# Optimization experiments

Hardware: AMD Instinct MI355X
Metric: run time of the kernel (lower is better)

The kernel has to match this reference:

```python
import jax, jax.numpy as jnp
from jax import lax
import numpy as np

B, T, UMAX, D = 32, 128, 64, 512
U1 = UMAX + 1
BLANK = D - 1  # blank=-1 -> last vocab slot
NEG = -1e30    # finite -inf surrogate (keeps logaddexp grads NaN-free)


def setup_inputs() -> dict:
    key = jax.random.key(0)
    k1, k2, k3, k4 = jax.random.split(key, 4)
    logits = jax.random.normal(k1, (B, T, U1, D), dtype=jnp.float32)
    logit_lengths = jax.random.randint(k2, (B,), T // 2, T + 1, dtype=jnp.int32)
    target_lengths = jax.random.randint(k3, (B,), UMAX // 2, UMAX + 1, dtype=jnp.int32)
    targets = jax.random.randint(k4, (B, UMAX), 0, D - 1, dtype=jnp.int32)  # never blank
    return {"logits": logits, "logit_lengths": logit_lengths,
            "target_lengths": target_lengths, "targets": targets}


def _transducer_costs(log_probs, logit_lengths, target_lengths, targets):
    """RNN-T alpha DP; costs[b] = -(alpha[T_b-1, U_b] + lp_blank[T_b-1, U_b])."""
    b, t_max, u1, d = log_probs.shape
    lp_blank = log_probs[..., BLANK]                                   # [B,T,U1]
    tgt_pad = jnp.concatenate([targets, jnp.zeros((b, 1), targets.dtype)], axis=1)  # [B,U1]
    lp_emit = jnp.take_along_axis(log_probs, tgt_pad[:, None, :, None], axis=3)[..., 0]  # [B,T,U1]
    u_idx = jnp.arange(u1)
    # emit transitions only exist for u < target_length (masks padded labels too)
    lp_emit = jnp.where(u_idx[None, None, :] < target_lengths[:, None, None], lp_emit, NEG)

    # alpha[0, u] = cumsum of emit log-probs along u
    row0 = jnp.concatenate(
        [jnp.zeros((b, 1), jnp.float32), jnp.cumsum(lp_emit[:, 0, :-1], axis=1)], axis=1)

    def row_step(prev_row, xs):
        lpb_prev, lpe = xs                      # both [B,U1]
        skip = prev_row + lpb_prev              # alpha[t-1,u] + blank(t-1,u)

        def inner(a_left, xu):
            s_u, e_um1 = xu                      # skip[:,u], lp_emit[:,t,u-1]
            a = jnp.logaddexp(s_u, a_left + e_um1)
            return a, a

        a0 = skip[:, 0]
        _, rest = lax.scan(inner, a0,
                           (jnp.moveaxis(skip[:, 1:], 1, 0),
                            jnp.moveaxis(lpe[:, :-1], 1, 0)))
        row = jnp.concatenate([a0[:, None], jnp.moveaxis(rest, 0, 1)], axis=1)
        return row, row

    xs = (jnp.moveaxis(lp_blank[:, :-1, :], 1, 0),   # blank at row t-1
          jnp.moveaxis(lp_emit[:, 1:, :], 1, 0))     # emit at row t
    _, rows = lax.scan(row_step, row0, xs)
    alpha = jnp.concatenate([row0[:, None, :], jnp.moveaxis(rows, 0, 1)], axis=1)  # [B,T,U1]

    bi = jnp.arange(b)
    tf = logit_lengths - 1
    uf = target_lengths
    return -(alpha[bi, tf, uf] + lp_blank[bi, tf, uf])


def reference(logits, logit_lengths, target_lengths, targets):
    lp = jax.nn.log_softmax(logits, axis=-1)
    return _transducer_costs(lp, logit_lengths, target_lengths, targets)
```

## Files before the change

### kernel.cpp

```cpp
#include <hip/hip_runtime.h>

#define BQ 32
#define TQ 128
#define U1Q 65
#define UMAXQ 64
#define DQ 512
#define SLAB (TQ * U1Q)
#define NCELLS (BQ * SLAB)
#define NEGQ (-1e30f)
#define L2E 1.4426950408889634f
#define LN2F 0.6931471805599453f

typedef float f4 __attribute__((ext_vector_type(4)));

#define EXP2(x) __builtin_amdgcn_exp2f(x)
#define LOG2(x) __builtin_amdgcn_logf(x)

__device__ __forceinline__ float logadd2(float x, float y) {
    float mx = fmaxf(x, y);
    float d  = fminf(x, y) - mx;
    return mx + LOG2(1.0f + EXP2(d));
}

__global__ __launch_bounds__(512) void lse_k(const float* __restrict__ logits,
                                             const int* __restrict__ targets,
                                             const int* __restrict__ llen,
                                             const int* __restrict__ tlen,
                                             float* __restrict__ ws) {
    int wid  = (blockIdx.x * 512 + threadIdx.x) >> 6;
    int lane = threadIdx.x & 63;
    int h = lane >> 3;
    int i = lane & 7;
    int r = wid * 8 + h;

    int b = r / SLAB;
    int q = r - b * SLAB;
    int t = q / U1Q;
    int u = q - t * U1Q;
    int tl = tlen[b];
    if (t >= llen[b] || u > tl) return;

    const f4* rp = (const f4*)(logits + (size_t)r * DQ) + i;
    f4 w0 = rp[0],   w1 = rp[8],   w2 = rp[16],  w3 = rp[24],
       w4 = rp[32],  w5 = rp[40],  w6 = rp[48],  w7 = rp[56],
       w8 = rp[64],  w9 = rp[72],  wA = rp[80],  wB = rp[88],
       wC = rp[96],  wD = rp[104], wE = rp[112], wF = rp[120];

#define SUM4(v) (EXP2((v).x * L2E) + EXP2((v).y * L2E) + \
                 EXP2((v).z * L2E) + EXP2((v).w * L2E))
    float s0 = (SUM4(w0) + SUM4(w1)) + (SUM4(w2) + SUM4(w3));
    float s1 = (SUM4(w4) + SUM4(w5)) + (SUM4(w6) + SUM4(w7));
    float s2 = (SUM4(w8) + SUM4(w9)) + (SUM4(wA) + SUM4(wB));
    float s3 = (SUM4(wC) + SUM4(wD)) + (SUM4(wE) + SUM4(wF));
    float s = (s0 + s1) + (s2 + s3);
#pragma unroll
    for (int d = 1; d <= 4; d <<= 1) s += __shfl_xor(s, d, 64);

    float l2s = LOG2(s);
    float* wb = ws + (size_t)b * 2 * SLAB;

    if (i == 7) wb[q] = fmaf(wF.w, L2E, -l2s);

    int tgt = targets[b * UMAXQ + (u < UMAXQ ? u : UMAXQ - 1)];
    int itgt = (tgt >> 2) & 7;
    if (i == itgt) {
        int ktgt = tgt >> 5, jt = tgt & 3;
        f4 c = w0;
        if (ktgt == 1)  c = w1;
        if (ktgt == 2)  c = w2;
        if (ktgt == 3)  c = w3;
        if (ktgt == 4)  c = w4;
        if (ktgt == 5)  c = w5;
        if (ktgt == 6)  c = w6;
        if (ktgt == 7)  c = w7;
        if (ktgt == 8)  c = w8;
        if (ktgt == 9)  c = w9;
        if (ktgt == 10) c = wA;
        if (ktgt == 11) c = wB;
        if (ktgt == 12) c = wC;
        if (ktgt == 13) c = wD;
        if (ktgt == 14) c = wE;
        if (ktgt == 15) c = wF;
        float val = (jt == 0) ? c.x : ((jt == 1) ? c.y : ((jt == 2) ? c.z : c.w));
        wb[SLAB + q] = (u < tl) ? fmaf(val, L2E, -l2s) : NEGQ;
    }
}

__global__ __launch_bounds__(512) void dp_k(const float* __restrict__ ws,
                                            const int* __restrict__ llen,
                                            const int* __restrict__ tlen,
                                            float* __restrict__ out) {
    __shared__ float S[2 * SLAB];
    int b   = blockIdx.x;
    int tid = threadIdx.x;

    int tf = llen[b] - 1;
    int uf = tlen[b];

    const f4* srcB = (const f4*)(ws + (size_t)b * 2 * SLAB);
    const f4* srcE = srcB + SLAB / 4;
    f4* dstB = (f4*)S;
    f4* dstE = (f4*)(S + SLAB);
    int nb4 = ((tf + 1) * U1Q + 3) >> 2;
    for (int idx = tid; idx < nb4; idx += 512) {
        dstB[idx] = srcB[idx];
        dstE[idx] = srcE[idx];
    }
    __syncthreads();
    if (tid >= 64) return;

    int lane = tid;
    const float* SB = S;
    const float* SE = S + SLAB;

    int kmax = tf + uf;

    float a   = (lane == 0) ? 0.0f : NEGQ;
    float a64 = NEGQ;
    int um1 = (lane > 0) ? lane - 1 : 0;

    auto LB = [&](int k) { int t = k - lane - 1; t = t < 0 ? 0 : (t > TQ - 1 ? TQ - 1 : t);
                           return SB[t * U1Q + lane]; };
    auto LE = [&](int k) { int t = k - lane;     t = t < 0 ? 0 : (t > TQ - 1 ? TQ - 1 : t);
                           return SE[t * U1Q + um1]; };
    auto LB6 = [&](int k) { int t = k - 65; t = t < 0 ? 0 : (t > TQ - 1 ? TQ - 1 : t);
                            return SB[t * U1Q + 64]; };
    auto LE6 = [&](int k) { int t = k - 64; t = t < 0 ? 0 : (t > TQ - 1 ? TQ - 1 : t);
                            return SE[t * U1Q + 63]; };

#define STEP(kk, lbv, lev, lb6v, le6v) do {                                  \
    int k_ = (kk); int t = k_ - lane;                                        \
    float A   = (t >= 1) ? (a + (lbv)) : NEGQ;                               \
    float ash = __shfl_up(a, 1, 64);                                         \
    float Bv  = (lane >= 1 && t >= 0) ? (ash + (lev)) : NEGQ;                \
    float a63 = __shfl(a, 63, 64);                                           \
    float anew = logadd2(A, Bv);                                             \
    int t64 = k_ - 64;                                                       \
    float A64 = (t64 >= 1) ? (a64 + (lb6v)) : NEGQ;                          \
    float B64 = (t64 >= 0) ? (a63 + (le6v)) : NEGQ;                          \
    a64 = (t64 >= 0) ? logadd2(A64, B64) : NEGQ;                             \
    a = anew;                                                                \
} while (0)

    float lbA = LB(1), leA = LE(1), lb6A = LB6(1), le6A = LE6(1);
    float lbB = LB(2), leB = LE(2), lb6B = LB6(2), le6B = LE6(2);
    float lbC = LB(3), leC = LE(3), lb6C = LB6(3), le6C = LE6(3);
    float lbD = LB(4), leD = LE(4), lb6D = LB6(4), le6D = LE6(4);

    int k = 1;
    for (; k + 3 <= kmax; k += 4) {
        STEP(k,     lbA, leA, lb6A, le6A); lbA = LB(k + 4); leA = LE(k + 4); lb6A = LB6(k + 4); le6A = LE6(k + 4);
        STEP(k + 1, lbB, leB, lb6B, le6B); lbB = LB(k + 5); leB = LE(k + 5); lb6B = LB6(k + 5); le6B = LE6(k + 5);
        STEP(k + 2, lbC, leC, lb6C, le6C); lbC = LB(k + 6); leC = LE(k + 6); lb6C = LB6(k + 6); le6C = LE6(k + 6);
        STEP(k + 3, lbD, leD, lb6D, le6D); lbD = LB(k + 7); leD = LE(k + 7); lb6D = LB6(k + 7); le6D = LE6(k + 7);
    }
    if (k <= kmax) { STEP(k, lbA, leA, lb6A, le6A); k++; }
    if (k <= kmax) { STEP(k, lbB, leB, lb6B, le6B); k++; }
    if (k <= kmax) { STEP(k, lbC, leC, lb6C, le6C); k++; }

    float alpha_f = (uf >= 64) ? a64 : __shfl(a, uf, 64);
    if (lane == 0) out[b] = -(alpha_f + SB[tf * U1Q + uf]) * LN2F;
}

extern "C" void kernel_launch(void* const* d_in, const int* in_sizes, int n_in,
                              void* d_out, int out_size, void* d_ws, size_t ws_size,
                              hipStream_t stream) {
    const float* logits  = (const float*)d_in[0];
    const int*   llen    = (const int*)d_in[1];
    const int*   tlen    = (const int*)d_in[2];
    const int*   targets = (const int*)d_in[3];
    float*       out     = (float*)d_out;
    float*       ws      = (float*)d_ws;

    int blocks = NCELLS / 64;
    lse_k<<<blocks, 512, 0, stream>>>(logits, targets, llen, tlen, ws);
    dp_k<<<BQ, 512, 0, stream>>>(ws, llen, tlen, out);
}
```

Baseline: 83.32 us.

## Precompute alpha column zero via prefix scan and pad slab for branchless DP

Column u=0 of alpha is now computed up front as a wavefront prefix sum of blank log-probs. The 64 lanes then only need to cover u=1..64, which removes the separate a64 tracking, the extra shuffle and the second logadd each diagonal step. The workspace and shared-memory layouts are padded to width 66 with a NEG guard region, so out-of-range loads return NEG and the per-step validity selects can go away. In exchange the LSE kernel writes extra padding and shared memory grows slightly. Since the DP is a latency-bound serial loop, cutting per-step work should shorten the critical path.

```diff
diff --git a/kernel.cpp b/kernel.cpp
--- a/kernel.cpp
+++ b/kernel.cpp
@@ -6,6 +6,10 @@
 #define UMAXQ 64
 #define DQ 512
 #define SLAB (TQ * U1Q)
+#define W66 66
+#define WS66 (TQ * W66)
+#define GR 68
+#define SLABSZ (GR + TQ * W66)
 #define NCELLS (BQ * SLAB)
 #define NEGQ (-1e30f)
 #define L2E 1.4426950408889634f
@@ -57,14 +61,19 @@
     for (int d = 1; d <= 4; d <<= 1) s += __shfl_xor(s, d, 64);
 
     float l2s = LOG2(s);
-    float* wb = ws + (size_t)b * 2 * SLAB;
+    float* wb = ws + (size_t)b * 2 * WS66;
+    int q66 = t * W66 + u;
 
-    if (i == 7) wb[q] = fmaf(wF.w, L2E, -l2s);
+    if (i == 7) {
+        wb[q66] = fmaf(wF.w, L2E, -l2s);
+        wb[t * W66 + 65]        = NEGQ;
+        wb[WS66 + t * W66 + 65] = NEGQ;
+    }
 
-    int tgt = targets[b * UMAXQ + (u < UMAXQ ? u : UMAXQ - 1)];
-    int itgt = (tgt >> 2) & 7;
+    int tg = targets[b * UMAXQ + (u < UMAXQ ? u : UMAXQ - 1)];
+    int itgt = (tg >> 2) & 7;
     if (i == itgt) {
-        int ktgt = tgt >> 5, jt = tgt & 3;
+        int ktgt = tg >> 5, jt = tg & 3;
         f4 c = w0;
         if (ktgt == 1)  c = w1;
         if (ktgt == 2)  c = w2;
@@ -82,7 +91,7 @@
         if (ktgt == 14) c = wE;
         if (ktgt == 15) c = wF;
         float val = (jt == 0) ? c.x : ((jt == 1) ? c.y : ((jt == 2) ? c.z : c.w));
-        wb[SLAB + q] = (u < tl) ? fmaf(val, L2E, -l2s) : NEGQ;
+        wb[WS66 + q66] = (u < tl) ? fmaf(val, L2E, -l2s) : NEGQ;
     }
 }
 
@@ -90,76 +99,83 @@
                                             const int* __restrict__ llen,
                                             const int* __restrict__ tlen,
                                             float* __restrict__ out) {
-    __shared__ float S[2 * SLAB];
+    __shared__ float S[2 * SLABSZ + 132];
     int b   = blockIdx.x;
     int tid = threadIdx.x;
 
     int tf = llen[b] - 1;
     int uf = tlen[b];
+    int kmax = tf + uf;
 
-    const f4* srcB = (const f4*)(ws + (size_t)b * 2 * SLAB);
-    const f4* srcE = srcB + SLAB / 4;
-    f4* dstB = (f4*)S;
-    f4* dstE = (f4*)(S + SLAB);
-    int nb4 = ((tf + 1) * U1Q + 3) >> 2;
+    float* SB  = S;
+    float* SE  = S + SLABSZ;
+    float* s0p = S + 2 * SLABSZ;
+
+    const f4* srcB = (const f4*)(ws + (size_t)b * 2 * WS66);
+    const f4* srcE = srcB + WS66 / 4;
+    f4* dstB = (f4*)SB + GR / 4;
+    f4* dstE = (f4*)SE + GR / 4;
+    int nb4 = ((tf + 1) * W66 + 3) >> 2;
     for (int idx = tid; idx < nb4; idx += 512) {
         dstB[idx] = srcB[idx];
         dstE[idx] = srcE[idx];
     }
+    if (tid < GR) { SB[tid] = NEGQ; SE[tid] = NEGQ; }
     __syncthreads();
     if (tid >= 64) return;
 
     int lane = tid;
-    const float* SB = S;
-    const float* SE = S + SLAB;
 
-    int kmax = tf + uf;
+    {
+        float x1 = (lane <= tf) ? SB[GR + lane * W66] : 0.0f;
+        float p1 = x1;
+#pragma unroll
+        for (int d = 1; d <= 32; d <<= 1) { float o = __shfl_up(p1, d, 64); if (lane >= d) p1 += o; }
+        float tot = __shfl(p1, 63, 64);
+        int t2 = lane + 64;
+        float x2 = (t2 <= tf) ? SB[GR + t2 * W66] : 0.0f;
+        float p2 = x2;
+#pragma unroll
+        for (int d = 1; d <= 32; d <<= 1) { float o = __shfl_up(p2, d, 64); if (lane >= d) p2 += o; }
+        if (lane == 0) s0p[0] = 0.0f;
+        s0p[lane + 1] = p1;
+        s0p[65 + lane] = tot + p2;
+    }
 
-    float a   = (lane == 0) ? 0.0f : NEGQ;
-    float a64 = NEGQ;
-    int um1 = (lane > 0) ? lane - 1 : 0;
+    float a = NEGQ;
 
-    auto LB = [&](int k) { int t = k - lane - 1; t = t < 0 ? 0 : (t > TQ - 1 ? TQ - 1 : t);
-                           return SB[t * U1Q + lane]; };
-    auto LE = [&](int k) { int t = k - lane;     t = t < 0 ? 0 : (t > TQ - 1 ? TQ - 1 : t);
-                           return SE[t * U1Q + um1]; };
-    auto LB6 = [&](int k) { int t = k - 65; t = t < 0 ? 0 : (t > TQ - 1 ? TQ - 1 : t);
-                            return SB[t * U1Q + 64]; };
-    auto LE6 = [&](int k) { int t = k - 64; t = t < 0 ? 0 : (t > TQ - 1 ? TQ - 1 : t);
-                            return SE[t * U1Q + 63]; };
+    auto LB = [&](int k) { int rb = k - lane - 2; rb = rb < -1 ? -1 : (rb > TQ - 1 ? TQ - 1 : rb);
+                           return SB[GR + rb * W66 + lane + 1]; };
+    auto LE = [&](int k) { int te = k - lane - 1; te = te < -1 ? -1 : (te > TQ - 1 ? TQ - 1 : te);
+                           return SE[GR + te * W66 + lane]; };
+    auto S0 = [&](int k) { int j = k - 1; j = j > 127 ? 127 : j; return s0p[j]; };
 
-#define STEP(kk, lbv, lev, lb6v, le6v) do {                                  \
-    int k_ = (kk); int t = k_ - lane;                                        \
-    float A   = (t >= 1) ? (a + (lbv)) : NEGQ;                               \
+#define STEP(lbv, lev, s0v) do {                                             \
     float ash = __shfl_up(a, 1, 64);                                         \
-    float Bv  = (lane >= 1 && t >= 0) ? (ash + (lev)) : NEGQ;                \
-    float a63 = __shfl(a, 63, 64);                                           \
-    float anew = logadd2(A, Bv);                                             \
-    int t64 = k_ - 64;                                                       \
-    float A64 = (t64 >= 1) ? (a64 + (lb6v)) : NEGQ;                          \
-    float B64 = (t64 >= 0) ? (a63 + (le6v)) : NEGQ;                          \
-    a64 = (t64 >= 0) ? logadd2(A64, B64) : NEGQ;                             \
-    a = anew;                                                                \
+    ash = (lane == 0) ? (s0v) : ash;                                         \
+    float A = a + (lbv);                                                     \
+    float B = ash + (lev);                                                   \
+    a = logadd2(A, B);                                                       \
 } while (0)
 
-    float lbA = LB(1), leA = LE(1), lb6A = LB6(1), le6A = LE6(1);
-    float lbB = LB(2), leB = LE(2), lb6B = LB6(2), le6B = LE6(2);
-    float lbC = LB(3), leC = LE(3), lb6C = LB6(3), le6C = LE6(3);
-    float lbD = LB(4), leD = LE(4), lb6D = LB6(4), le6D = LE6(4);
+    float lbA = LB(1), leA = LE(1), sA = S0(1);
+    float lbB = LB(2), leB = LE(2), sB = S0(2);
+    float lbC = LB(3), leC = LE(3), sC = S0(3);
+    float lbD = LB(4), leD = LE(4), sD = S0(4);
 
     int k = 1;
     for (; k + 3 <= kmax; k += 4) {
-        STEP(k,     lbA, leA, lb6A, le6A); lbA = LB(k + 4); leA = LE(k + 4); lb6A = LB6(k + 4); le6A = LE6(k + 4);
-        STEP(k + 1, lbB, leB, lb6B, le6B); lbB = LB(k + 5); leB = LE(k + 5); lb6B = LB6(k + 5); le6B = LE6(k + 5);
-        STEP(k + 2, lbC, leC, lb6C, le6C); lbC = LB(k + 6); leC = LE(k + 6); lb6C = LB6(k + 6); le6C = LE6(k + 6);
-        STEP(k + 3, lbD, leD, lb6D, le6D); lbD = LB(k + 7); leD = LE(k + 7); lb6D = LB6(k + 7); le6D = LE6(k + 7);
+        STEP(lbA, leA, sA); lbA = LB(k + 4); leA = LE(k + 4); sA = S0(k + 4);
+        STEP(lbB, leB, sB); lbB = LB(k + 5); leB = LE(k + 5); sB = S0(k + 5);
+        STEP(lbC, leC, sC); lbC = LB(k + 6); leC = LE(k + 6); sC = S0(k + 6);
+        STEP(lbD, leD, sD); lbD = LB(k + 7); leD = LE(k + 7); sD = S0(k + 7);
     }
-    if (k <= kmax) { STEP(k, lbA, leA, lb6A, le6A); k++; }
-    if (k <= kmax) { STEP(k, lbB, leB, lb6B, le6B); k++; }
-    if (k <= kmax) { STEP(k, lbC, leC, lb6C, le6C); k++; }
+    if (k <= kmax) { STEP(lbA, leA, sA); k++; }
+    if (k <= kmax) { STEP(lbB, leB, sB); k++; }
+    if (k <= kmax) { STEP(lbC, leC, sC); k++; }
 
-    float alpha_f = (uf >= 64) ? a64 : __shfl(a, uf, 64);
-    if (lane == 0) out[b] = -(alpha_f + SB[tf * U1Q + uf]) * LN2F;
+    float alpha_f = __shfl(a, uf - 1, 64);
+    if (lane == 0) out[b] = -(alpha_f + SB[GR + tf * W66 + uf]) * LN2F;
 }
 
 extern "C" void kernel_launch(void* const* d_in, const int* in_sizes, int n_in,
```

Result: faster. 73.33 us (-12.0%).
